# Kernel tuning notes

Hardware: AMD Instinct MI355X
Metric: run time of the kernel (lower is better)

## Reference

```python
import jax, jax.numpy as jnp
import numpy as np
import math

N_HEAD = 16

def _rope_cos_sin(T, head_dim):
    # thetas[i] = 10000 ** (-2*(i-1)/dim) for i = 1..dim/2  ->  exponent -2*j/dim, j=0..dim/2-1
    j = jnp.arange(head_dim // 2, dtype=jnp.float32)
    theta = jnp.power(10000.0, -2.0 * j / head_dim)          # [d/2]
    t = jnp.arange(T, dtype=jnp.float32)                      # [T]
    ang = t[:, None] * theta[None, :]                         # [T, d/2]
    return jnp.cos(ang), jnp.sin(ang)

def _apply_rope(u, cos, sin):
    # u: [B,H,T,d]; interleaved complex rotation over pairs (u[...,2i], u[...,2i+1])
    B, H, T, d = u.shape
    u = u.reshape(B, H, T, d // 2, 2)
    u0, u1 = u[..., 0], u[..., 1]
    r0 = u0 * cos - u1 * sin
    r1 = u0 * sin + u1 * cos
    return jnp.stack([r0, r1], axis=-1).reshape(B, H, T, d)

def setup_inputs() -> dict:
    key = jax.random.key(0)
    ks = jax.random.split(key, 9)
    C = 1024
    s = 1.0 / math.sqrt(C)
    return {
        "x": jax.random.normal(ks[0], (4, 2048, C), dtype=jnp.float32),
        "wq": jax.random.normal(ks[1], (C, C), dtype=jnp.float32) * s,
        "bq": jax.random.normal(ks[2], (C,), dtype=jnp.float32) * s,
        "wk": jax.random.normal(ks[3], (C, C), dtype=jnp.float32) * s,
        "bk": jax.random.normal(ks[4], (C,), dtype=jnp.float32) * s,
        "wv": jax.random.normal(ks[5], (C, C), dtype=jnp.float32) * s,
        "bv": jax.random.normal(ks[6], (C,), dtype=jnp.float32) * s,
        "wp": jax.random.normal(ks[7], (C, C), dtype=jnp.float32) * s,
        "bp": jax.random.normal(ks[8], (C,), dtype=jnp.float32) * s,
    }

def reference(x, wq, bq, wk, bk, wv, bv, wp, bp):
    B, T, C = x.shape
    H = N_HEAD
    d = C // H
    def proj(w, b):
        # nn.Linear: x @ w.T + b, then split heads -> [B,H,T,d]
        return (jnp.einsum('btc,oc->bto', x, w) + b).reshape(B, T, H, d).transpose(0, 2, 1, 3)
    q, k, v = proj(wq, bq), proj(wk, bk), proj(wv, bv)
    cos, sin = _rope_cos_sin(T, d)
    q = _apply_rope(q, cos, sin)
    k = _apply_rope(k, cos, sin)
    att = jnp.einsum('bhqd,bhkd->bhqk', q, k) * (1.0 / math.sqrt(d))  # [B,H,T,T]
    causal = jnp.tril(jnp.ones((T, T), dtype=bool))
    att = jnp.where(causal, att, jnp.finfo(att.dtype).min)
    att = jax.nn.softmax(att, axis=-1)
    y = jnp.einsum('bhqk,bhkd->bhqd', att, v)                         # [B,H,T,d]
    y = y.transpose(0, 2, 1, 3).reshape(B, T, C)
    return jnp.einsum('btc,oc->bto', y, wp) + bp
```

## Files before the change

kernel.cpp:

```cpp
#include <hip/hip_runtime.h>

typedef __attribute__((ext_vector_type(8))) __bf16 bf16x8;
typedef __attribute__((ext_vector_type(4))) float f32x4;
typedef __attribute__((ext_vector_type(16))) float f32x16;
typedef unsigned short u16;

#define TSEQ   2048
#define NB     4
#define NHEAD  16
#define HDIM   64
#define CMODEL 1024
#define MTOK   (NB*TSEQ)

__device__ __forceinline__ u16 f2bf(float x){
  unsigned u = __float_as_uint(x);
  u += 0x7fffu + ((u >> 16) & 1u);
  return (u16)(u >> 16);
}

__device__ __forceinline__ unsigned cvtpk(float lo, float hi){
  unsigned r;
  asm("v_cvt_pk_bf16_f32 %0, %1, %2" : "=v"(r) : "v"(lo), "v"(hi));
  return r;
}
__device__ __forceinline__ void plswap(unsigned &a, unsigned &b){
  asm volatile("v_permlane32_swap_b32 %0, %1" : "+v"(a), "+v"(b));
}

__device__ __forceinline__ void async16(const void* g, const u16* lds_base){
  __builtin_amdgcn_global_load_lds(
      (const __attribute__((address_space(1))) unsigned*)(uintptr_t)g,
      (__attribute__((address_space(3))) unsigned*)(unsigned)(uintptr_t)lds_base,
      16, 0, 0);
}

__global__ void cast_bf16_kernel(const float* __restrict__ src, u16* __restrict__ dst, int n4){
  int i = blockIdx.x * blockDim.x + threadIdx.x;
  int stride = gridDim.x * blockDim.x;
  for (; i < n4; i += stride){
    float4 v = ((const float4*)src)[i];
    ((ushort4*)dst)[i] = make_ushort4(f2bf(v.x), f2bf(v.y), f2bf(v.z), f2bf(v.w));
  }
}

__global__ void cast4_bf16_kernel(const float* __restrict__ s0, const float* __restrict__ s1,
                                  const float* __restrict__ s2, const float* __restrict__ s3,
                                  u16* __restrict__ d0, u16* __restrict__ d1,
                                  u16* __restrict__ d2, u16* __restrict__ d3, int n4){
  int which = blockIdx.y;
  const float* s = (which==0)?s0:(which==1)?s1:(which==2)?s2:s3;
  u16* d        = (which==0)?d0:(which==1)?d1:(which==2)?d2:d3;
  int i = blockIdx.x * blockDim.x + threadIdx.x;
  int stride = gridDim.x * blockDim.x;
  for (; i < n4; i += stride){
    float4 v = ((const float4*)s)[i];
    ((ushort4*)d)[i] = make_ushort4(f2bf(v.x), f2bf(v.y), f2bf(v.z), f2bf(v.w));
  }
}

__global__ void rope_table_kernel(float2* __restrict__ rope){
  int i = blockIdx.x * blockDim.x + threadIdx.x;
  if (i >= TSEQ * (HDIM/2)) return;
  int t = i >> 5, j = i & 31;
  float theta = exp2f(-(float)j * (13.287712379549449f / 32.f));
  float ang = (float)t * theta;
  rope[i] = make_float2(cosf(ang), sinf(ang));
}

__device__ __forceinline__ void gemm128_mainloop(
    const u16* __restrict__ A, const u16* __restrict__ B,
    int m0, int n0, int K, u16* sA, u16* sB, f32x4 acc[4][4])
{
  const int tid = threadIdx.x;
  const int w = tid >> 6, lane = tid & 63;
  const int ln = lane & 15, g = lane >> 4;
  const int wm = w >> 1, wn = w & 1;

  const f32x4 zero = {0.f, 0.f, 0.f, 0.f};
#pragma unroll
  for (int mt = 0; mt < 4; ++mt)
#pragma unroll
    for (int nt = 0; nt < 4; ++nt) acc[mt][nt] = zero;

  for (int k0 = 0; k0 < K; k0 += 64){
    __syncthreads();
#pragma unroll
    for (int i = 0; i < 4; ++i){
      int c = i*256 + tid;
      int r = c >> 3, sl = c & 7;
      int ks = sl ^ (r & 7);
      async16(A + (size_t)(m0 + r)*K + k0 + ks*8, sA + (size_t)(i*256 + w*64)*8);
      async16(B + (size_t)(n0 + r)*K + k0 + ks*8, sB + (size_t)(i*256 + w*64)*8);
    }
    __syncthreads();

#pragma unroll
    for (int kk = 0; kk < 2; ++kk){
      bf16x8 af[4], bfr[4];
#pragma unroll
      for (int mt = 0; mt < 4; ++mt){
        int row = wm*64 + mt*16 + ln;
        int sl = (kk*4 + g) ^ (row & 7);
        af[mt] = *(const bf16x8*)&sA[row*64 + sl*8];
      }
#pragma unroll
      for (int nt = 0; nt < 4; ++nt){
        int row = wn*64 + nt*16 + ln;
        int sl = (kk*4 + g) ^ (row & 7);
        bfr[nt] = *(const bf16x8*)&sB[row*64 + sl*8];
      }
      __builtin_amdgcn_s_setprio(1);
#pragma unroll
      for (int mt = 0; mt < 4; ++mt)
#pragma unroll
        for (int nt = 0; nt < 4; ++nt)
          acc[mt][nt] = __builtin_amdgcn_mfma_f32_16x16x32_bf16(af[mt], bfr[nt], acc[mt][nt], 0, 0, 0);
      __builtin_amdgcn_s_setprio(0);
    }
  }
}

#define SCQ 0.18033688011112042f

__global__ __launch_bounds__(256) void gemm_qkv_kernel(
    const u16* __restrict__ xb,
    const u16* __restrict__ wqb, const u16* __restrict__ wkb, const u16* __restrict__ wvb,
    const float* __restrict__ bq, const float* __restrict__ bk, const float* __restrict__ bv,
    const float2* __restrict__ rope,
    u16* __restrict__ Qh, u16* __restrict__ Kh, u16* __restrict__ Vt)
{
  __shared__ u16 sA[128*64];
  __shared__ u16 sB[128*64];
  const int z = blockIdx.z;
  const u16*  W    = (z == 0) ? wqb : (z == 1) ? wkb : wvb;
  const float* bias = (z == 0) ? bq  : (z == 1) ? bk  : bv;
  const int m0 = blockIdx.y * 128, n0 = blockIdx.x * 128;

  f32x4 acc[4][4];
  gemm128_mainloop(xb, W, m0, n0, CMODEL, sA, sB, acc);

  const int tid = threadIdx.x, w = tid >> 6, lane = tid & 63;
  const int ln = lane & 15, g = lane >> 4;
  const int wm = w >> 1, wn = w & 1;

#pragma unroll
  for (int mt = 0; mt < 4; ++mt){
#pragma unroll
    for (int nt = 0; nt < 4; ++nt){
      int o  = n0 + wn*64 + nt*16 + ln;
      float bb = bias[o];
      int h  = o >> 6;
      int dd = o & 63;
      if (z < 2){
        int j = dd >> 1;
        u16* dst = (z == 0) ? Qh : Kh;
        float qs = (z == 0) ? SCQ : 1.0f;
#pragma unroll
        for (int rr = 0; rr < 4; ++rr){
          int t  = m0 + wm*64 + mt*16 + g*4 + rr;
          int b  = t >> 11, tt = t & (TSEQ-1);
          float v  = acc[mt][nt][rr] + bb;
          float pv = __shfl_xor(v, 1);
          float2 cs = rope[tt*32 + j];
          float out = ((o & 1) == 0) ? (v*cs.x - pv*cs.y) : (pv*cs.y + v*cs.x);
          dst[(size_t)((b*NHEAD + h)*TSEQ + tt)*HDIM + dd] = f2bf(out * qs);
        }
      } else {
        int t0 = m0 + wm*64 + mt*16 + g*4;
        int b  = t0 >> 11, tt0 = t0 & (TSEQ-1);
        u16 pk[4];
#pragma unroll
        for (int rr = 0; rr < 4; ++rr) pk[rr] = f2bf(acc[mt][nt][rr] + bb);
        *(ushort4*)&Vt[(size_t)((b*NHEAD + h)*HDIM + dd)*TSEQ + tt0] =
            make_ushort4(pk[0], pk[1], pk[2], pk[3]);
      }
    }
  }
}

__global__ __launch_bounds__(256) void attn_kernel(
    const u16* __restrict__ Qh, const u16* __restrict__ Kh,
    const u16* __restrict__ Vt, u16* __restrict__ yb)
{
  __shared__ u16 sK[2][64*64];
  __shared__ u16 sV[2][64*64];

  const int tid = threadIdx.x, w = tid >> 6, lane = tid & 63;
  const int ln = lane & 31, hi = lane >> 5;

  const int bid = blockIdx.x;
  const int xcd = bid & 7, s = bid >> 3;
  const int qt  = 15 - (s >> 3);
  const int bh  = xcd * 8 + (s & 7);
  const int b   = bh >> 4, h = bh & (NHEAD-1);

  const u16* Qbase = Qh + (size_t)bh * TSEQ * HDIM;
  const u16* Kbase = Kh + (size_t)bh * TSEQ * HDIM;
  const u16* Vbase = Vt + (size_t)bh * HDIM * TSEQ;

  const int r0   = qt*128 + w*32;
  const int jtb  = 2*qt + 1;
  const int jtw  = 2*qt + (w >> 1);
  const int wodd = w & 1;

  const int swz = ln & 7;
  const f32x16 zero16 = {0,0,0,0,0,0,0,0,0,0,0,0,0,0,0,0};

  const int c0r = tid >> 3,          c0p = tid & 7;
  const int c1r = (256+tid) >> 3,    c1p = (256+tid) & 7;
  const u16* kp0 = Kbase + (size_t)c0r*HDIM + ((c0p ^ (c0r&7))<<3);
  const u16* kp1 = Kbase + (size_t)c1r*HDIM + ((c1p ^ (c1r&7))<<3);
  const u16* vp0 = Vbase + (size_t)c0r*TSEQ + ((c0p ^ (c0r&7))<<3);
  const u16* vp1 = Vbase + (size_t)c1r*TSEQ + ((c1p ^ (c1r&7))<<3);
  const unsigned dst0 = (unsigned)(w*64)*8;
  const unsigned dst1 = (unsigned)(256 + w*64)*8;

  unsigned offd[4];
#pragma unroll
  for (int d = 0; d < 4; ++d) offd[d] = ((unsigned)((2*d + hi) ^ swz)) * 8;
  const unsigned rowl = (unsigned)ln * 64;
  const unsigned rowh = rowl + 32*64;

  bf16x8 qf[4];
#pragma unroll
  for (int ds = 0; ds < 4; ++ds)
    qf[ds] = *(const bf16x8*)&Qbase[(size_t)(r0 + ln)*HDIM + ds*16 + hi*8];

  f32x16 yacc0 = zero16, yacc1 = zero16;
  float m2 = -1e30f, lp = 0.f;

  int buf = 0;
  async16(kp0, sK[0] + dst0);
  async16(kp1, sK[0] + dst1);
  async16(vp0, sV[0] + dst0);
  async16(vp1, sV[0] + dst1);

#pragma unroll 1
  for (int jt = 0; jt <= jtb; ++jt){
    __syncthreads();
    if (jt < jtb){
      const size_t ko = (size_t)(jt+1) * (64*HDIM);
      const size_t vo = (size_t)(jt+1) * 64;
      u16* sKb = sK[buf^1]; u16* sVb = sV[buf^1];
      async16(kp0 + ko, sKb + dst0);
      async16(kp1 + ko, sKb + dst1);
      async16(vp0 + vo, sVb + dst0);
      async16(vp1 + vo, sVb + dst1);
    }

    if (jt <= jtw){
      const u16* sKb = sK[buf];
      const u16* sVb = sV[buf];
      const bool full1 = (jt < jtw) || wodd;

      f32x16 p0 = zero16, p1 = zero16;
      __builtin_amdgcn_s_setprio(1);
#pragma unroll
      for (int ds = 0; ds < 4; ++ds){
        bf16x8 k0 = *(const bf16x8*)&sKb[rowl + offd[ds]];
        p0 = __builtin_amdgcn_mfma_f32_32x32x16_bf16(k0, qf[ds], p0, 0, 0, 0);
      }
      if (full1){
#pragma unroll
        for (int ds = 0; ds < 4; ++ds){
          bf16x8 k1 = *(const bf16x8*)&sKb[rowh + offd[ds]];
          p1 = __builtin_amdgcn_mfma_f32_32x32x16_bf16(k1, qf[ds], p1, 0, 0, 0);
        }
      }
      __builtin_amdgcn_s_setprio(0);

      if (jt == jtw){
#pragma unroll
        for (int r = 0; r < 16; ++r){
          int k0r = (r&3) + 8*(r>>2) + 4*hi;
          bool cut = k0r > ln;
          if (!wodd){ if (cut) p0[r] = -1e30f; }
          else      { if (cut) p1[r] = -1e30f; }
        }
      }

      float lm = p0[0];
#pragma unroll
      for (int r = 1; r < 16; ++r) lm = fmaxf(lm, p0[r]);
      if (full1){
#pragma unroll
        for (int r = 0; r < 16; ++r) lm = fmaxf(lm, p1[r]);
      }

      if (__any(lm - m2 > 8.0f)){
        float lmp = __shfl_xor(lm, 32);
        float mn  = fmaxf(m2, fmaxf(lm, lmp));
        float scl = exp2f(m2 - mn);
        m2 = mn;
        lp *= scl;
#pragma unroll
        for (int r = 0; r < 16; ++r){
          float sr = __shfl(scl, (r&3) + 8*(r>>2) + 4*hi);
          yacc0[r] *= sr; yacc1[r] *= sr;
        }
      }

      float ts = 0.f;
#pragma unroll
      for (int r = 0; r < 16; ++r){ p0[r] = exp2f(p0[r] - m2); ts += p0[r]; }
      if (full1){
#pragma unroll
        for (int r = 0; r < 16; ++r){ p1[r] = exp2f(p1[r] - m2); ts += p1[r]; }
      }
      lp += ts;

      bf16x8 pa[4];
      {
        union { unsigned u[4]; bf16x8 v; } f0, f1;
        unsigned A0 = cvtpk(p0[0], p0[1]),  B0 = cvtpk(p0[2], p0[3]);
        unsigned A1 = cvtpk(p0[4], p0[5]),  B1 = cvtpk(p0[6], p0[7]);
        plswap(A0, A1); plswap(B0, B1);
        f0.u[0]=A0; f0.u[1]=B0; f0.u[2]=A1; f0.u[3]=B1;  pa[0]=f0.v;
        unsigned A2 = cvtpk(p0[8], p0[9]),  B2 = cvtpk(p0[10], p0[11]);
        unsigned A3 = cvtpk(p0[12], p0[13]),B3 = cvtpk(p0[14], p0[15]);
        plswap(A2, A3); plswap(B2, B3);
        f1.u[0]=A2; f1.u[1]=B2; f1.u[2]=A3; f1.u[3]=B3;  pa[1]=f1.v;
      }
      if (full1){
        union { unsigned u[4]; bf16x8 v; } f2, f3;
        unsigned A4 = cvtpk(p1[0], p1[1]),  B4 = cvtpk(p1[2], p1[3]);
        unsigned A5 = cvtpk(p1[4], p1[5]),  B5 = cvtpk(p1[6], p1[7]);
        plswap(A4, A5); plswap(B4, B5);
        f2.u[0]=A4; f2.u[1]=B4; f2.u[2]=A5; f2.u[3]=B5;  pa[2]=f2.v;
        unsigned A6 = cvtpk(p1[8], p1[9]),  B6 = cvtpk(p1[10], p1[11]);
        unsigned A7 = cvtpk(p1[12], p1[13]),B7 = cvtpk(p1[14], p1[15]);
        plswap(A6, A7); plswap(B6, B7);
        f3.u[0]=A6; f3.u[1]=B6; f3.u[2]=A7; f3.u[3]=B7;  pa[3]=f3.v;
      }

      __builtin_amdgcn_s_setprio(1);
#pragma unroll
      for (int st = 0; st < 2; ++st){
        bf16x8 v0 = *(const bf16x8*)&sVb[rowl + offd[st]];
        bf16x8 v1 = *(const bf16x8*)&sVb[rowh + offd[st]];
        yacc0 = __builtin_amdgcn_mfma_f32_32x32x16_bf16(pa[st], v0, yacc0, 0, 0, 0);
        yacc1 = __builtin_amdgcn_mfma_f32_32x32x16_bf16(pa[st], v1, yacc1, 0, 0, 0);
      }
      if (full1){
#pragma unroll
        for (int st = 2; st < 4; ++st){
          bf16x8 v0 = *(const bf16x8*)&sVb[rowl + offd[st]];
          bf16x8 v1 = *(const bf16x8*)&sVb[rowh + offd[st]];
          yacc0 = __builtin_amdgcn_mfma_f32_32x32x16_bf16(pa[st], v0, yacc0, 0, 0, 0);
          yacc1 = __builtin_amdgcn_mfma_f32_32x32x16_bf16(pa[st], v1, yacc1, 0, 0, 0);
        }
      }
      __builtin_amdgcn_s_setprio(0);
    }
    buf ^= 1;
  }

  float lpf = lp + __shfl_xor(lp, 32);
  float inv = 1.0f / lpf;
#pragma unroll
  for (int r = 0; r < 16; ++r){
    int q = (r&3) + 8*(r>>2) + 4*hi;
    float ir = __shfl(inv, q);
    int tt = r0 + q;
    size_t rowoff = (size_t)(b*TSEQ + tt)*CMODEL + h*HDIM;
    yb[rowoff + ln]      = f2bf(yacc0[r] * ir);
    yb[rowoff + 32 + ln] = f2bf(yacc1[r] * ir);
  }
}

__global__ __launch_bounds__(256) void gemm_proj_kernel(
    const u16* __restrict__ yb, const u16* __restrict__ wpb,
    const float* __restrict__ bp, float* __restrict__ out)
{
  __shared__ u16 sA[128*64];
  __shared__ u16 sB[128*64];
  const int m0 = blockIdx.y * 128, n0 = blockIdx.x * 128;
  f32x4 acc[4][4];
  gemm128_mainloop(yb, wpb, m0, n0, CMODEL, sA, sB, acc);

  const int tid = threadIdx.x, w = tid >> 6, lane = tid & 63;
  const int ln = lane & 15, g = lane >> 4;
  const int wm = w >> 1, wn = w & 1;
#pragma unroll
  for (int mt = 0; mt < 4; ++mt)
#pragma unroll
    for (int nt = 0; nt < 4; ++nt){
      int o = n0 + wn*64 + nt*16 + ln;
      float bb = bp[o];
#pragma unroll
      for (int rr = 0; rr < 4; ++rr){
        int t = m0 + wm*64 + mt*16 + g*4 + rr;
        out[(size_t)t*CMODEL + o] = acc[mt][nt][rr] + bb;
      }
    }
}

extern "C" void kernel_launch(void* const* d_in, const int* in_sizes, int n_in,
                              void* d_out, int out_size, void* d_ws, size_t ws_size,
                              hipStream_t stream)
{
  const float* x  = (const float*)d_in[0];
  const float* wq = (const float*)d_in[1];
  const float* bq = (const float*)d_in[2];
  const float* wk = (const float*)d_in[3];
  const float* bk = (const float*)d_in[4];
  const float* wv = (const float*)d_in[5];
  const float* bv = (const float*)d_in[6];
  const float* wp = (const float*)d_in[7];
  const float* bp = (const float*)d_in[8];

  char* ws = (char*)d_ws;
  u16*    xb   = (u16*)   (ws + 0);
  u16*    wqb  = (u16*)   (ws + 16777216);
  u16*    wkb  = (u16*)   (ws + 18874368);
  u16*    wvb  = (u16*)   (ws + 20971520);
  u16*    wpb  = (u16*)   (ws + 23068672);
  float2* rope = (float2*)(ws + 25165824);
  u16*    Qh   = (u16*)   (ws + 25690112);
  u16*    Kh   = (u16*)   (ws + 42467328);
  u16*    Vt   = (u16*)   (ws + 59244544);
  u16*    yb   = (u16*)   (ws + 76021760);

  cast_bf16_kernel<<<2048, 256, 0, stream>>>(x,  xb,  MTOK*CMODEL/4);
  cast4_bf16_kernel<<<dim3(256, 4), 256, 0, stream>>>(wq, wk, wv, wp, wqb, wkb, wvb, wpb,
                                                      CMODEL*CMODEL/4);
  rope_table_kernel<<<(TSEQ*(HDIM/2) + 255)/256, 256, 0, stream>>>(rope);

  gemm_qkv_kernel<<<dim3(CMODEL/128, MTOK/128, 3), 256, 0, stream>>>(
      xb, wqb, wkb, wvb, bq, bk, bv, rope, Qh, Kh, Vt);

  attn_kernel<<<dim3(1024), 256, 0, stream>>>(Qh, Kh, Vt, yb);

  gemm_proj_kernel<<<dim3(CMODEL/128, MTOK/128), 256, 0, stream>>>(yb, wpb, bp, (float*)d_out);
}
```

Before: 213.4 us.

## Split attention into 64-row query tiles with two-wave blocks

The attention kernel now uses 128-thread blocks covering 64 query rows each, launched as 2048 blocks instead of 1024 blocks of 128 rows. This removes the idle waves that sat out the last causal tile, since every wave now works each iteration, and it gives finer-grained load balancing across the causal triangle. In exchange each K/V tile is loaded from global memory for half as many query rows, which doubles K/V traffic and the per-block loop overhead. The copy loop is rewritten so each thread issues four async loads per buffer.

```diff
diff --git a/kernel.cpp b/kernel.cpp
--- a/kernel.cpp
+++ b/kernel.cpp
@@ -178,7 +178,7 @@
   }
 }
 
-__global__ __launch_bounds__(256) void attn_kernel(
+__global__ __launch_bounds__(128) void attn_kernel(
     const u16* __restrict__ Qh, const u16* __restrict__ Kh,
     const u16* __restrict__ Vt, u16* __restrict__ yb)
 {
@@ -189,31 +189,27 @@
   const int ln = lane & 31, hi = lane >> 5;
 
   const int bid = blockIdx.x;
-  const int xcd = bid & 7, s = bid >> 3;
-  const int qt  = 15 - (s >> 3);
-  const int bh  = xcd * 8 + (s & 7);
+  const int t   = 31 - (bid >> 6);
+  const int bh  = (bid & 7) * 8 + ((bid >> 3) & 7);
   const int b   = bh >> 4, h = bh & (NHEAD-1);
 
   const u16* Qbase = Qh + (size_t)bh * TSEQ * HDIM;
   const u16* Kbase = Kh + (size_t)bh * TSEQ * HDIM;
   const u16* Vbase = Vt + (size_t)bh * HDIM * TSEQ;
 
-  const int r0   = qt*128 + w*32;
-  const int jtb  = 2*qt + 1;
-  const int jtw  = 2*qt + (w >> 1);
-  const int wodd = w & 1;
+  const int r0 = t*64 + w*32;
 
   const int swz = ln & 7;
   const f32x16 zero16 = {0,0,0,0,0,0,0,0,0,0,0,0,0,0,0,0};
 
-  const int c0r = tid >> 3,          c0p = tid & 7;
-  const int c1r = (256+tid) >> 3,    c1p = (256+tid) & 7;
-  const u16* kp0 = Kbase + (size_t)c0r*HDIM + ((c0p ^ (c0r&7))<<3);
-  const u16* kp1 = Kbase + (size_t)c1r*HDIM + ((c1p ^ (c1r&7))<<3);
-  const u16* vp0 = Vbase + (size_t)c0r*TSEQ + ((c0p ^ (c0r&7))<<3);
-  const u16* vp1 = Vbase + (size_t)c1r*TSEQ + ((c1p ^ (c1r&7))<<3);
-  const unsigned dst0 = (unsigned)(w*64)*8;
-  const unsigned dst1 = (unsigned)(256 + w*64)*8;
+  const u16* kp[4]; const u16* vp[4]; unsigned dstc[4];
+#pragma unroll
+  for (int i = 0; i < 4; ++i){
+    int c = i*128 + tid, r = c >> 3, pc = c & 7;
+    kp[i]   = Kbase + (size_t)r*HDIM + ((pc ^ (r&7))<<3);
+    vp[i]   = Vbase + (size_t)r*TSEQ + ((pc ^ (r&7))<<3);
+    dstc[i] = (unsigned)(i*128 + w*64)*8;
+  }
 
   unsigned offd[4];
 #pragma unroll
@@ -230,128 +226,129 @@
   float m2 = -1e30f, lp = 0.f;
 
   int buf = 0;
-  async16(kp0, sK[0] + dst0);
-  async16(kp1, sK[0] + dst1);
-  async16(vp0, sV[0] + dst0);
-  async16(vp1, sV[0] + dst1);
+#pragma unroll
+  for (int i = 0; i < 4; ++i){
+    async16(kp[i], sK[0] + dstc[i]);
+    async16(vp[i], sV[0] + dstc[i]);
+  }
 
 #pragma unroll 1
-  for (int jt = 0; jt <= jtb; ++jt){
+  for (int jt = 0; jt <= t; ++jt){
     __syncthreads();
-    if (jt < jtb){
+    if (jt < t){
       const size_t ko = (size_t)(jt+1) * (64*HDIM);
       const size_t vo = (size_t)(jt+1) * 64;
       u16* sKb = sK[buf^1]; u16* sVb = sV[buf^1];
-      async16(kp0 + ko, sKb + dst0);
-      async16(kp1 + ko, sKb + dst1);
-      async16(vp0 + vo, sVb + dst0);
-      async16(vp1 + vo, sVb + dst1);
-    }
-
-    if (jt <= jtw){
-      const u16* sKb = sK[buf];
-      const u16* sVb = sV[buf];
-      const bool full1 = (jt < jtw) || wodd;
-
-      f32x16 p0 = zero16, p1 = zero16;
-      __builtin_amdgcn_s_setprio(1);
+#pragma unroll
+      for (int i = 0; i < 4; ++i){
+        async16(kp[i] + ko, sKb + dstc[i]);
+        async16(vp[i] + vo, sVb + dstc[i]);
+      }
+    }
+
+    const u16* sKb = sK[buf];
+    const u16* sVb = sV[buf];
+    const bool full1 = (jt < t) || w;
+
+    f32x16 p0 = zero16, p1 = zero16;
+    __builtin_amdgcn_s_setprio(1);
+#pragma unroll
+    for (int ds = 0; ds < 4; ++ds){
+      bf16x8 k0 = *(const bf16x8*)&sKb[rowl + offd[ds]];
+      p0 = __builtin_amdgcn_mfma_f32_32x32x16_bf16(k0, qf[ds], p0, 0, 0, 0);
+    }
+    if (full1){
 #pragma unroll
       for (int ds = 0; ds < 4; ++ds){
-        bf16x8 k0 = *(const bf16x8*)&sKb[rowl + offd[ds]];
-        p0 = __builtin_amdgcn_mfma_f32_32x32x16_bf16(k0, qf[ds], p0, 0, 0, 0);
-      }
-      if (full1){
-#pragma unroll
-        for (int ds = 0; ds < 4; ++ds){
-          bf16x8 k1 = *(const bf16x8*)&sKb[rowh + offd[ds]];
-          p1 = __builtin_amdgcn_mfma_f32_32x32x16_bf16(k1, qf[ds], p1, 0, 0, 0);
-        }
-      }
-      __builtin_amdgcn_s_setprio(0);
-
-      if (jt == jtw){
-#pragma unroll
-        for (int r = 0; r < 16; ++r){
-          int k0r = (r&3) + 8*(r>>2) + 4*hi;
-          bool cut = k0r > ln;
-          if (!wodd){ if (cut) p0[r] = -1e30f; }
-          else      { if (cut) p1[r] = -1e30f; }
-        }
-      }
-
-      float lm = p0[0];
-#pragma unroll
-      for (int r = 1; r < 16; ++r) lm = fmaxf(lm, p0[r]);
-      if (full1){
-#pragma unroll
-        for (int r = 0; r < 16; ++r) lm = fmaxf(lm, p1[r]);
-      }
-
-      if (__any(lm - m2 > 8.0f)){
-        float lmp = __shfl_xor(lm, 32);
-        float mn  = fmaxf(m2, fmaxf(lm, lmp));
-        float scl = exp2f(m2 - mn);
-        m2 = mn;
-        lp *= scl;
-#pragma unroll
-        for (int r = 0; r < 16; ++r){
-          float sr = __shfl(scl, (r&3) + 8*(r>>2) + 4*hi);
-          yacc0[r] *= sr; yacc1[r] *= sr;
-        }
-      }
-
-      float ts = 0.f;
-#pragma unroll
-      for (int r = 0; r < 16; ++r){ p0[r] = exp2f(p0[r] - m2); ts += p0[r]; }
-      if (full1){
-#pragma unroll
-        for (int r = 0; r < 16; ++r){ p1[r] = exp2f(p1[r] - m2); ts += p1[r]; }
-      }
-      lp += ts;
-
-      bf16x8 pa[4];
-      {
-        union { unsigned u[4]; bf16x8 v; } f0, f1;
-        unsigned A0 = cvtpk(p0[0], p0[1]),  B0 = cvtpk(p0[2], p0[3]);
-        unsigned A1 = cvtpk(p0[4], p0[5]),  B1 = cvtpk(p0[6], p0[7]);
-        plswap(A0, A1); plswap(B0, B1);
-        f0.u[0]=A0; f0.u[1]=B0; f0.u[2]=A1; f0.u[3]=B1;  pa[0]=f0.v;
-        unsigned A2 = cvtpk(p0[8], p0[9]),  B2 = cvtpk(p0[10], p0[11]);
-        unsigned A3 = cvtpk(p0[12], p0[13]),B3 = cvtpk(p0[14], p0[15]);
-        plswap(A2, A3); plswap(B2, B3);
-        f1.u[0]=A2; f1.u[1]=B2; f1.u[2]=A3; f1.u[3]=B3;  pa[1]=f1.v;
-      }
-      if (full1){
-        union { unsigned u[4]; bf16x8 v; } f2, f3;
-        unsigned A4 = cvtpk(p1[0], p1[1]),  B4 = cvtpk(p1[2], p1[3]);
-        unsigned A5 = cvtpk(p1[4], p1[5]),  B5 = cvtpk(p1[6], p1[7]);
-        plswap(A4, A5); plswap(B4, B5);
-        f2.u[0]=A4; f2.u[1]=B4; f2.u[2]=A5; f2.u[3]=B5;  pa[2]=f2.v;
-        unsigned A6 = cvtpk(p1[8], p1[9]),  B6 = cvtpk(p1[10], p1[11]);
-        unsigned A7 = cvtpk(p1[12], p1[13]),B7 = cvtpk(p1[14], p1[15]);
-        plswap(A6, A7); plswap(B6, B7);
-        f3.u[0]=A6; f3.u[1]=B6; f3.u[2]=A7; f3.u[3]=B7;  pa[3]=f3.v;
-      }
-
-      __builtin_amdgcn_s_setprio(1);
-#pragma unroll
-      for (int st = 0; st < 2; ++st){
+        bf16x8 k1 = *(const bf16x8*)&sKb[rowh + offd[ds]];
+        p1 = __builtin_amdgcn_mfma_f32_32x32x16_bf16(k1, qf[ds], p1, 0, 0, 0);
+      }
+    }
+    __builtin_amdgcn_s_setprio(0);
+
+    if (jt == t){
+#pragma unroll
+      for (int r = 0; r < 16; ++r){
+        int k0r = (r&3) + 8*(r>>2) + 4*hi;
+        bool cut = k0r > ln;
+        if (!w){ if (cut) p0[r] = -1e30f; }
+        else   { if (cut) p1[r] = -1e30f; }
+      }
+    }
+
+    float lm = p0[0];
+#pragma unroll
+    for (int r = 1; r < 16; ++r) lm = fmaxf(lm, p0[r]);
+    if (full1){
+#pragma unroll
+      for (int r = 0; r < 16; ++r) lm = fmaxf(lm, p1[r]);
+    }
+
+    if (__any(lm - m2 > 8.0f)){
+      float lmp = __shfl_xor(lm, 32);
+      float mn  = fmaxf(m2, fmaxf(lm, lmp));
+      float scl = exp2f(m2 - mn);
+      m2 = mn;
+      lp *= scl;
+#pragma unroll
+      for (int r = 0; r < 16; ++r){
+        float sr = __shfl(scl, (r&3) + 8*(r>>2) + 4*hi);
+        yacc0[r] *= sr; yacc1[r] *= sr;
+      }
+    }
+
+    float ts = 0.f;
+#pragma unroll
+    for (int r = 0; r < 16; ++r){ p0[r] = exp2f(p0[r] - m2); ts += p0[r]; }
+    if (full1){
+#pragma unroll
+      for (int r = 0; r < 16; ++r){ p1[r] = exp2f(p1[r] - m2); ts += p1[r]; }
+    }
+    lp += ts;
+
+    bf16x8 pa[4];
+    {
+      union { unsigned u[4]; bf16x8 v; } f0, f1;
+      unsigned A0 = cvtpk(p0[0], p0[1]),  B0 = cvtpk(p0[2], p0[3]);
+      unsigned A1 = cvtpk(p0[4], p0[5]),  B1 = cvtpk(p0[6], p0[7]);
+      plswap(A0, A1); plswap(B0, B1);
+      f0.u[0]=A0; f0.u[1]=B0; f0.u[2]=A1; f0.u[3]=B1;  pa[0]=f0.v;
+      unsigned A2 = cvtpk(p0[8], p0[9]),  B2 = cvtpk(p0[10], p0[11]);
+      unsigned A3 = cvtpk(p0[12], p0[13]),B3 = cvtpk(p0[14], p0[15]);
+      plswap(A2, A3); plswap(B2, B3);
+      f1.u[0]=A2; f1.u[1]=B2; f1.u[2]=A3; f1.u[3]=B3;  pa[1]=f1.v;
+    }
+    if (full1){
+      union { unsigned u[4]; bf16x8 v; } f2, f3;
+      unsigned A4 = cvtpk(p1[0], p1[1]),  B4 = cvtpk(p1[2], p1[3]);
+      unsigned A5 = cvtpk(p1[4], p1[5]),  B5 = cvtpk(p1[6], p1[7]);
+      plswap(A4, A5); plswap(B4, B5);
+      f2.u[0]=A4; f2.u[1]=B4; f2.u[2]=A5; f2.u[3]=B5;  pa[2]=f2.v;
+      unsigned A6 = cvtpk(p1[8], p1[9]),  B6 = cvtpk(p1[10], p1[11]);
+      unsigned A7 = cvtpk(p1[12], p1[13]),B7 = cvtpk(p1[14], p1[15]);
+      plswap(A6, A7); plswap(B6, B7);
+      f3.u[0]=A6; f3.u[1]=B6; f3.u[2]=A7; f3.u[3]=B7;  pa[3]=f3.v;
+    }
+
+    __builtin_amdgcn_s_setprio(1);
+#pragma unroll
+    for (int st = 0; st < 2; ++st){
+      bf16x8 v0 = *(const bf16x8*)&sVb[rowl + offd[st]];
+      bf16x8 v1 = *(const bf16x8*)&sVb[rowh + offd[st]];
+      yacc0 = __builtin_amdgcn_mfma_f32_32x32x16_bf16(pa[st], v0, yacc0, 0, 0, 0);
+      yacc1 = __builtin_amdgcn_mfma_f32_32x32x16_bf16(pa[st], v1, yacc1, 0, 0, 0);
+    }
+    if (full1){
+#pragma unroll
+      for (int st = 2; st < 4; ++st){
         bf16x8 v0 = *(const bf16x8*)&sVb[rowl + offd[st]];
         bf16x8 v1 = *(const bf16x8*)&sVb[rowh + offd[st]];
         yacc0 = __builtin_amdgcn_mfma_f32_32x32x16_bf16(pa[st], v0, yacc0, 0, 0, 0);
         yacc1 = __builtin_amdgcn_mfma_f32_32x32x16_bf16(pa[st], v1, yacc1, 0, 0, 0);
       }
-      if (full1){
-#pragma unroll
-        for (int st = 2; st < 4; ++st){
-          bf16x8 v0 = *(const bf16x8*)&sVb[rowl + offd[st]];
-          bf16x8 v1 = *(const bf16x8*)&sVb[rowh + offd[st]];
-          yacc0 = __builtin_amdgcn_mfma_f32_32x32x16_bf16(pa[st], v0, yacc0, 0, 0, 0);
-          yacc1 = __builtin_amdgcn_mfma_f32_32x32x16_bf16(pa[st], v1, yacc1, 0, 0, 0);
-        }
-      }
-      __builtin_amdgcn_s_setprio(0);
-    }
+    }
+    __builtin_amdgcn_s_setprio(0);
+
     buf ^= 1;
   }
 
@@ -429,7 +426,7 @@
   gemm_qkv_kernel<<<dim3(CMODEL/128, MTOK/128, 3), 256, 0, stream>>>(
       xb, wqb, wkb, wvb, bq, bk, bv, rope, Qh, Kh, Vt);
 
-  attn_kernel<<<dim3(1024), 256, 0, stream>>>(Qh, Kh, Vt, yb);
+  attn_kernel<<<dim3(2048), 128, 0, stream>>>(Qh, Kh, Vt, yb);
 
   gemm_proj_kernel<<<dim3(CMODEL/128, MTOK/128), 256, 0, stream>>>(yb, wpb, bp, (float*)d_out);
 }
```

Measured after the change: 216.8 us. No clear change (+1.6%).

## Use 512-thread attention blocks with 256-row Q tiles and triple-buffered K/V prefetch

Applied to the files above, without the earlier changes.

The attention kernel now runs 8 waves per block, each block covering 256 query rows instead of 128. That halves the grid and doubles K/V reuse per shared-memory load. The K/V staging moves from double to triple buffering with a prefetch distance of two tiles, and __syncthreads is replaced by explicit vmcnt waits plus s_barrier. The aim is to hide global load latency and cut redundant K/V traffic, at the cost of more LDS per block, coarser causal load balance across blocks and fewer blocks overall.

```diff
diff --git a/kernel.cpp b/kernel.cpp
--- a/kernel.cpp
+++ b/kernel.cpp
@@ -178,49 +178,44 @@
   }
 }
 
-__global__ __launch_bounds__(256) void attn_kernel(
+__global__ __launch_bounds__(512, 4) void attn_kernel(
     const u16* __restrict__ Qh, const u16* __restrict__ Kh,
     const u16* __restrict__ Vt, u16* __restrict__ yb)
 {
-  __shared__ u16 sK[2][64*64];
-  __shared__ u16 sV[2][64*64];
+  __shared__ u16 sK[3][64*64];
+  __shared__ u16 sV[3][64*64];
 
   const int tid = threadIdx.x, w = tid >> 6, lane = tid & 63;
   const int ln = lane & 31, hi = lane >> 5;
 
   const int bid = blockIdx.x;
-  const int xcd = bid & 7, s = bid >> 3;
-  const int qt  = 15 - (s >> 3);
-  const int bh  = xcd * 8 + (s & 7);
+  const int s   = 7 - (bid >> 6);
+  const int bh  = (bid & 7) * 8 + ((bid >> 3) & 7);
   const int b   = bh >> 4, h = bh & (NHEAD-1);
 
   const u16* Qbase = Qh + (size_t)bh * TSEQ * HDIM;
   const u16* Kbase = Kh + (size_t)bh * TSEQ * HDIM;
   const u16* Vbase = Vt + (size_t)bh * HDIM * TSEQ;
 
-  const int r0   = qt*128 + w*32;
-  const int jtb  = 2*qt + 1;
-  const int jtw  = 2*qt + (w >> 1);
-  const int wodd = w & 1;
+  const int cr = tid >> 3, cs = tid & 7;
+  const u16* kp = Kbase + (size_t)cr*HDIM + ((cs ^ (cr&7))<<3);
+  const u16* vp = Vbase + (size_t)cr*TSEQ + ((cs ^ (cr&7))<<3);
+  const unsigned dstw = (unsigned)(w*64)*8;
 
   const int swz = ln & 7;
-  const f32x16 zero16 = {0,0,0,0,0,0,0,0,0,0,0,0,0,0,0,0};
-
-  const int c0r = tid >> 3,          c0p = tid & 7;
-  const int c1r = (256+tid) >> 3,    c1p = (256+tid) & 7;
-  const u16* kp0 = Kbase + (size_t)c0r*HDIM + ((c0p ^ (c0r&7))<<3);
-  const u16* kp1 = Kbase + (size_t)c1r*HDIM + ((c1p ^ (c1r&7))<<3);
-  const u16* vp0 = Vbase + (size_t)c0r*TSEQ + ((c0p ^ (c0r&7))<<3);
-  const u16* vp1 = Vbase + (size_t)c1r*TSEQ + ((c1p ^ (c1r&7))<<3);
-  const unsigned dst0 = (unsigned)(w*64)*8;
-  const unsigned dst1 = (unsigned)(256 + w*64)*8;
-
   unsigned offd[4];
 #pragma unroll
   for (int d = 0; d < 4; ++d) offd[d] = ((unsigned)((2*d + hi) ^ swz)) * 8;
   const unsigned rowl = (unsigned)ln * 64;
   const unsigned rowh = rowl + 32*64;
 
+  const f32x16 zero16 = {0,0,0,0,0,0,0,0,0,0,0,0,0,0,0,0};
+  const int wodd = w & 1;
+
+  const int r0  = s*256 + w*32;
+  const int jtb = 4*s + 3;
+  const int jtw = 4*s + (w >> 1);
+
   bf16x8 qf[4];
 #pragma unroll
   for (int ds = 0; ds < 4; ++ds)
@@ -229,28 +224,26 @@
   f32x16 yacc0 = zero16, yacc1 = zero16;
   float m2 = -1e30f, lp = 0.f;
 
-  int buf = 0;
-  async16(kp0, sK[0] + dst0);
-  async16(kp1, sK[0] + dst1);
-  async16(vp0, sV[0] + dst0);
-  async16(vp1, sV[0] + dst1);
+  async16(kp,                   sK[0] + dstw);
+  async16(vp,                   sV[0] + dstw);
+  async16(kp + (size_t)64*HDIM, sK[1] + dstw);
+  async16(vp + 64,              sV[1] + dstw);
+  asm volatile("s_waitcnt vmcnt(2)" ::: "memory");
+  asm volatile("s_barrier" ::: "memory");
 
 #pragma unroll 1
   for (int jt = 0; jt <= jtb; ++jt){
-    __syncthreads();
-    if (jt < jtb){
-      const size_t ko = (size_t)(jt+1) * (64*HDIM);
-      const size_t vo = (size_t)(jt+1) * 64;
-      u16* sKb = sK[buf^1]; u16* sVb = sV[buf^1];
-      async16(kp0 + ko, sKb + dst0);
-      async16(kp1 + ko, sKb + dst1);
-      async16(vp0 + vo, sVb + dst0);
-      async16(vp1 + vo, sVb + dst1);
+    const bool st2 = (jt + 2 <= jtb);
+    if (st2){
+      const int nb = (jt + 2) % 3;
+      async16(kp + (size_t)(jt+2)*64*HDIM, sK[nb] + dstw);
+      async16(vp + (size_t)(jt+2)*64,      sV[nb] + dstw);
     }
 
     if (jt <= jtw){
-      const u16* sKb = sK[buf];
-      const u16* sVb = sV[buf];
+      const int cb = jt % 3;
+      const u16* sKb = sK[cb];
+      const u16* sVb = sV[cb];
       const bool full1 = (jt < jtw) || wodd;
 
       f32x16 p0 = zero16, p1 = zero16;
@@ -352,7 +345,10 @@
       }
       __builtin_amdgcn_s_setprio(0);
     }
-    buf ^= 1;
+
+    if (st2) asm volatile("s_waitcnt vmcnt(2)" ::: "memory");
+    else     asm volatile("s_waitcnt vmcnt(0)" ::: "memory");
+    asm volatile("s_barrier" ::: "memory");
   }
 
   float lpf = lp + __shfl_xor(lp, 32);
@@ -429,7 +425,7 @@
   gemm_qkv_kernel<<<dim3(CMODEL/128, MTOK/128, 3), 256, 0, stream>>>(
       xb, wqb, wkb, wvb, bq, bk, bv, rope, Qh, Kh, Vt);
 
-  attn_kernel<<<dim3(1024), 256, 0, stream>>>(Qh, Kh, Vt, yb);
+  attn_kernel<<<dim3(512), 512, 0, stream>>>(Qh, Kh, Vt, yb);
 
   gemm_proj_kernel<<<dim3(CMODEL/128, MTOK/128), 256, 0, stream>>>(yb, wpb, bp, (float*)d_out);
 }
```

Result: faster. 202.3 us (-5.2%).
